# Kernel optimization log

Hardware: AMD Instinct MI355X
Metric: run time of the kernel (lower is better)

The kernel has to match this reference:

```python
import jax, jax.numpy as jnp
import numpy as np

D_MODEL = 768
D_FF = 3072
N_HEADS = 12
HEAD_DIM = D_MODEL // N_HEADS
SUB_SCALE = 0.5
LN_EPS = 1e-5


def _layer_norm(x, g, b):
    mu = jnp.mean(x, axis=-1, keepdims=True)
    var = jnp.var(x, axis=-1, keepdims=True)
    return (x - mu) * jax.lax.rsqrt(var + LN_EPS) * g + b


def setup_inputs() -> dict:
    key = jax.random.key(0)
    ks = jax.random.split(key, 12)
    B, T = 1, 4096
    s = lambda fan_in: 1.0 / np.sqrt(fan_in)
    return {
        "x": jax.random.normal(ks[0], (B, T, D_MODEL), dtype=jnp.float32),
        "ln1_g": jnp.ones((D_MODEL,), jnp.float32),
        "ln1_b": jnp.zeros((D_MODEL,), jnp.float32),
        "ln2_g": jnp.ones((D_MODEL,), jnp.float32),
        "ln2_b": jnp.zeros((D_MODEL,), jnp.float32),
        "qkv_w": jax.random.normal(ks[1], (D_MODEL, 3 * D_MODEL), jnp.float32) * s(D_MODEL),
        "qkv_b": jnp.zeros((3 * D_MODEL,), jnp.float32),
        "out_w": jax.random.normal(ks[2], (D_MODEL, D_MODEL), jnp.float32) * s(D_MODEL),
        "out_b": jnp.zeros((D_MODEL,), jnp.float32),
        "fc1_w": jax.random.normal(ks[3], (D_MODEL, D_FF), jnp.float32) * s(D_MODEL),
        "fc1_b": jnp.zeros((D_FF,), jnp.float32),
        "fc2_w": jax.random.normal(ks[4], (D_FF, D_MODEL), jnp.float32) * s(D_FF),
        "fc2_b": jnp.zeros((D_MODEL,), jnp.float32),
    }


def reference(x, ln1_g, ln1_b, ln2_g, ln2_b, qkv_w, qkv_b, out_w, out_b,
              fc1_w, fc1_b, fc2_w, fc2_b):
    B, T, C = x.shape
    # --- attention sub-block ---
    h = _layer_norm(x, ln1_g, ln1_b) * SUB_SCALE
    qkv = h @ qkv_w + qkv_b                      # [B,T,3C]
    q, k, v = jnp.split(qkv, 3, axis=-1)
    split = lambda t: t.reshape(B, T, N_HEADS, HEAD_DIM).transpose(0, 2, 1, 3)
    q, k, v = split(q), split(k), split(v)       # [B,H,T,Hd]
    scores = jnp.einsum('bhqd,bhkd->bhqk', q, k) / jnp.sqrt(jnp.float32(HEAD_DIM))
    weights = jax.nn.softmax(scores, axis=-1)    # [B,H,T,T] (no mask, as in source)
    attn = jnp.einsum('bhqk,bhkd->bhqd', weights, v)
    attn = attn.transpose(0, 2, 1, 3).reshape(B, T, C)
    x = x + attn @ out_w + out_b
    # --- MLP sub-block ---
    h2 = _layer_norm(x, ln2_g, ln2_b) * SUB_SCALE
    h2 = jax.nn.gelu(h2 @ fc1_w + fc1_b, approximate=False)  # nn.GELU() = exact erf
    h2 = h2 @ fc2_w + fc2_b
    return x + h2
```

## Files before the change

kernel.cpp:

```cpp
#include <hip/hip_runtime.h>
#include <hip/hip_bf16.h>
#include <math.h>

#define TSEQ 4096
#define DMODEL 768
#define DFF 3072
#define NHEADS 12
#define HDIM 64

typedef __attribute__((ext_vector_type(8))) short short8;
typedef __attribute__((ext_vector_type(4))) short bf16x4;
typedef __attribute__((ext_vector_type(4))) float f32x4;
typedef unsigned short ushort;
typedef unsigned int uint;

typedef __attribute__((address_space(1))) ushort as1_ushort;
typedef __attribute__((address_space(3))) ushort as3_ushort;

__device__ __forceinline__ void gl_lds16(const ushort* g, const ushort* l) {
    __builtin_amdgcn_global_load_lds((as1_ushort*)(uintptr_t)g,
                                     (as3_ushort*)(uint)(uintptr_t)l, 16, 0, 0);
}

__device__ __forceinline__ ushort f2bf(float f) {
    union { float f; unsigned i; } c; c.f = f;
    unsigned x = c.i;
    unsigned r = x + 0x7FFFu + ((x >> 16) & 1u);
    return (ushort)(r >> 16);
}
__device__ __forceinline__ float asf(uint u) {
    union { unsigned i; float f; } c; c.i = u; return c.f;
}

__global__ __launch_bounds__(256) void ln_half_kernel(
    const float* __restrict__ x, const float* __restrict__ g,
    const float* __restrict__ b, ushort* __restrict__ out)
{
    int row = blockIdx.x;
    const float* xr = x + (size_t)row * DMODEL;
    float v[3];
    float s = 0.f, s2 = 0.f;
    #pragma unroll
    for (int i = 0; i < 3; i++) {
        v[i] = xr[threadIdx.x + 256 * i];
        s += v[i]; s2 += v[i] * v[i];
    }
    #pragma unroll
    for (int m = 1; m < 64; m <<= 1) { s += __shfl_xor(s, m, 64); s2 += __shfl_xor(s2, m, 64); }
    __shared__ float ss[4], ss2[4];
    int wid = threadIdx.x >> 6;
    if ((threadIdx.x & 63) == 0) { ss[wid] = s; ss2[wid] = s2; }
    __syncthreads();
    s = ss[0] + ss[1] + ss[2] + ss[3];
    s2 = ss2[0] + ss2[1] + ss2[2] + ss2[3];
    float mu = s * (1.f / DMODEL);
    float var = s2 * (1.f / DMODEL) - mu * mu;
    float rs = rsqrtf(var + 1e-5f);
    #pragma unroll
    for (int i = 0; i < 3; i++) {
        int c = threadIdx.x + 256 * i;
        float h = (v[i] - mu) * rs * g[c] + b[c];
        out[(size_t)row * DMODEL + c] = f2bf(h * 0.5f);
    }
}

__global__ __launch_bounds__(256) void transpose_cast_kernel(
    const float* __restrict__ in, ushort* __restrict__ out, int K, int N)
{
    __shared__ float tile[32][33];
    int k0 = blockIdx.x * 32, n0 = blockIdx.y * 32;
    int c = threadIdx.x & 31, r0 = threadIdx.x >> 5;
    #pragma unroll
    for (int i = 0; i < 4; i++) {
        int r = r0 + i * 8;
        tile[r][c] = in[(size_t)(k0 + r) * N + n0 + c];
    }
    __syncthreads();
    #pragma unroll
    for (int i = 0; i < 4; i++) {
        int r = r0 + i * 8;
        out[(size_t)(n0 + r) * K + k0 + c] = f2bf(tile[c][r]);
    }
}

template<int EPI>
__global__ __launch_bounds__(256) void gemm_kernel(
    const ushort* __restrict__ A, const ushort* __restrict__ Bt,
    const float* __restrict__ bias, const float* __restrict__ res,
    void* __restrict__ out, int M, int N, int K)
{
    __shared__ ushort As[3][128 * 32];
    __shared__ ushort Bs[3][128 * 32];
    int bm = blockIdx.x * 128, bn = blockIdx.y * 128;
    int tid = threadIdx.x;
    int wid = tid >> 6, lane = tid & 63;
    int wm = (wid >> 1) * 64, wn = (wid & 1) * 64;
    int lg = lane >> 4, lr = lane & 15;
    int srow = lane >> 2, scol = (lane & 3) * 8;
    f32x4 acc[4][4] = {};

    const ushort* ga0 = A  + (size_t)(bm + wid * 16 + srow) * K + scol;
    const ushort* ga1 = A  + (size_t)(bm + 64 + wid * 16 + srow) * K + scol;
    const ushort* gb0 = Bt + (size_t)(bn + wid * 16 + srow) * K + scol;
    const ushort* gb1 = Bt + (size_t)(bn + 64 + wid * 16 + srow) * K + scol;

    auto STAGE = [&](int t, int b) {
        int k0 = t << 5;
        gl_lds16(ga0 + k0, &As[b][wid * 512]);
        gl_lds16(ga1 + k0, &As[b][2048 + wid * 512]);
        gl_lds16(gb0 + k0, &Bs[b][wid * 512]);
        gl_lds16(gb1 + k0, &Bs[b][2048 + wid * 512]);
    };

    int nt = K >> 5;
    STAGE(0, 0);
    STAGE(1, 1);

    int cur = 0;
    for (int t = 0; t < nt; t++) {
        if (t + 1 < nt) { asm volatile("s_waitcnt vmcnt(4)" ::: "memory"); }
        else            { asm volatile("s_waitcnt vmcnt(0)" ::: "memory"); }
        __builtin_amdgcn_s_barrier();
        if (t + 2 < nt) STAGE(t + 2, cur == 0 ? 2 : cur - 1);
        short8 a[4], b[4];
        #pragma unroll
        for (int mi = 0; mi < 4; mi++) a[mi] = *(const short8*)&As[cur][(wm + mi * 16 + lr) * 32 + lg * 8];
        #pragma unroll
        for (int ni = 0; ni < 4; ni++) b[ni] = *(const short8*)&Bs[cur][(wn + ni * 16 + lr) * 32 + lg * 8];
        #pragma unroll
        for (int mi = 0; mi < 4; mi++)
            #pragma unroll
            for (int ni = 0; ni < 4; ni++)
                acc[mi][ni] = __builtin_amdgcn_mfma_f32_16x16x32_bf16(a[mi], b[ni], acc[mi][ni], 0, 0, 0);
        cur = (cur == 2) ? 0 : cur + 1;
    }

    #pragma unroll
    for (int mi = 0; mi < 4; mi++) {
        #pragma unroll
        for (int ni = 0; ni < 4; ni++) {
            int col = bn + wn + ni * 16 + lr;
            float bv = bias[col];
            #pragma unroll
            for (int r = 0; r < 4; r++) {
                int row = bm + wm + mi * 16 + lg * 4 + r;
                float v = acc[mi][ni][r] + bv;
                size_t idx = (size_t)row * N + col;
                if (EPI == 0) {
                    ((ushort*)out)[idx] = f2bf(v);
                } else if (EPI == 1) {
                    float gv = 0.5f * v * (1.f + erff(v * 0.70710678118f));
                    ((ushort*)out)[idx] = f2bf(gv);
                } else {
                    ((float*)out)[idx] = v + res[idx];
                }
            }
        }
    }
}

__global__ __launch_bounds__(512) void attn_kernel(
    const ushort* __restrict__ qkv, ushort* __restrict__ Opart, float* __restrict__ ml)
{
    int h = blockIdx.y;
    int qb = blockIdx.x;
    int split = blockIdx.z;
    __shared__ ushort Ks[2][64 * 64];
    __shared__ ushort Vt[2][64 * 72];
    __shared__ ushort Ps[128 * 72];
    int tid = threadIdx.x, wid = tid >> 6, lane = tid & 63;
    int lg = lane >> 4, lr = lane & 15;
    const float C1 = 0.18033688011112042f;
    const float KC = 12.0f * C1;
    const size_t sbase = (size_t)split * 1024 * 2304;

    {
        int row = tid >> 2, cc = (tid & 3) * 16;
        const ushort* src = qkv + (size_t)(qb * 128 + row) * 2304 + h * HDIM + cc;
        *(short8*)&Ps[row * 72 + cc]     = *(const short8*)src;
        *(short8*)&Ps[row * 72 + cc + 8] = *(const short8*)(src + 8);
    }
    int prow = (wid * 16 + lr) * 72;
    short8 qf0 = *(const short8*)&Ps[prow + lg * 8];
    short8 qf1 = *(const short8*)&Ps[prow + 32 + lg * 8];

    short8 vone;
    #pragma unroll
    for (int i = 0; i < 8; i++) vone[i] = (short)0x3F80;

    int krow = tid >> 3;
    int kunit = (tid & 7) ^ (krow & 7);
    const ushort* kg = qkv + sbase + (size_t)krow * 2304 + DMODEL + h * HDIM + kunit * 8;
    int va_ = tid & 31, dg = tid >> 5;
    const ushort* vg = qkv + sbase + (size_t)(2 * va_) * 2304 + 2 * DMODEL + h * HDIM + dg * 4;

    bf16x4 nva = *(const bf16x4*)vg;
    bf16x4 nvb = *(const bf16x4*)(vg + 2304);
    gl_lds16(kg, &Ks[0][tid * 8]);
    #pragma unroll
    for (int i = 0; i < 4; i++) {
        uint pk = ((uint)(ushort)nva[i]) | (((uint)(ushort)nvb[i]) << 16);
        *(uint*)&Vt[0][(dg * 4 + i) * 72 + va_ * 2] = pk;
    }

    f32x4 o[4] = {};
    f32x4 o5 = {};
    const int NT = 16;
    int x7 = lr & 7;

    for (int kt = 0; kt < NT; kt++) {
        int cur = kt & 1, nb = cur ^ 1;
        bool pf = (kt + 1 < NT);
        __syncthreads();
        if (pf) {
            size_t off = (size_t)(kt + 1) * 64 * 2304;
            nva = *(const bf16x4*)(vg + off);
            nvb = *(const bf16x4*)(vg + off + 2304);
            gl_lds16(kg + off, &Ks[nb][tid * 8]);
        }

        f32x4 st[4] = {};
        #pragma unroll
        for (int ki = 0; ki < 4; ki++) {
            const ushort* kr = &Ks[cur][(ki * 16 + lr) * 64];
            short8 k0 = *(const short8*)&kr[(lg ^ x7) * 8];
            short8 k1 = *(const short8*)&kr[((4 + lg) ^ x7) * 8];
            st[ki] = __builtin_amdgcn_mfma_f32_16x16x32_bf16(k0, qf0, st[ki], 0, 0, 0);
            st[ki] = __builtin_amdgcn_mfma_f32_16x16x32_bf16(k1, qf1, st[ki], 0, 0, 0);
        }

        #pragma unroll
        for (int ki = 0; ki < 4; ki++)
            #pragma unroll
            for (int r = 0; r < 4; r++)
                st[ki][r] = exp2f(st[ki][r] * C1 - KC);

        #pragma unroll
        for (int ki = 0; ki < 4; ki++) {
            uint d0, d1;
            asm("v_cvt_pk_bf16_f32 %0, %1, %2" : "=v"(d0) : "v"(st[ki][0]), "v"(st[ki][1]));
            asm("v_cvt_pk_bf16_f32 %0, %1, %2" : "=v"(d1) : "v"(st[ki][2]), "v"(st[ki][3]));
            *(uint*)&Ps[prow + ki * 16 + lg * 4]     = d0;
            *(uint*)&Ps[prow + ki * 16 + lg * 4 + 2] = d1;
        }

        short8 pa0 = *(const short8*)&Ps[prow + lg * 8];
        short8 pa1 = *(const short8*)&Ps[prow + 32 + lg * 8];
        o5 = __builtin_amdgcn_mfma_f32_16x16x32_bf16(pa0, vone, o5, 0, 0, 0);
        o5 = __builtin_amdgcn_mfma_f32_16x16x32_bf16(pa1, vone, o5, 0, 0, 0);
        #pragma unroll
        for (int ni = 0; ni < 4; ni++) {
            const ushort* vr = &Vt[cur][(ni * 16 + lr) * 72];
            short8 b0 = *(const short8*)&vr[lg * 8];
            short8 b1 = *(const short8*)&vr[32 + lg * 8];
            o[ni] = __builtin_amdgcn_mfma_f32_16x16x32_bf16(pa0, b0, o[ni], 0, 0, 0);
            o[ni] = __builtin_amdgcn_mfma_f32_16x16x32_bf16(pa1, b1, o[ni], 0, 0, 0);
        }

        if (pf) {
            #pragma unroll
            for (int i = 0; i < 4; i++) {
                uint pk = ((uint)(ushort)nva[i]) | (((uint)(ushort)nvb[i]) << 16);
                *(uint*)&Vt[nb][(dg * 4 + i) * 72 + va_ * 2] = pk;
            }
        }
    }

    if (lr == 0) {
        #pragma unroll
        for (int r = 0; r < 4; r++) {
            int q = qb * 128 + wid * 16 + lg * 4 + r;
            ml[((size_t)split * NHEADS + h) * TSEQ + q] = o5[r];
        }
    }
    #pragma unroll
    for (int ni = 0; ni < 4; ni++)
        #pragma unroll
        for (int r = 0; r < 4; r++) {
            int qrow = qb * 128 + wid * 16 + lg * 4 + r;
            int dcol = ni * 16 + lr;
            Opart[((size_t)split * TSEQ + qrow) * DMODEL + h * HDIM + dcol] = f2bf(o[ni][r]);
        }
}

__global__ __launch_bounds__(256) void attn_combine_kernel(
    const ushort* __restrict__ Opart, const float* __restrict__ ml,
    ushort* __restrict__ attnb)
{
    int gid = blockIdx.x * 256 + threadIdx.x;
    int q = gid / 192;
    int c = (gid - q * 192) * 4;
    int hh = c >> 6;
    float denom = 0.f;
    float a0 = 0.f, a1 = 0.f, a2 = 0.f, a3 = 0.f;
    #pragma unroll
    for (int s = 0; s < 4; s++) {
        denom += ml[((size_t)s * NHEADS + hh) * TSEQ + q];
        uint2 ov = *(const uint2*)&Opart[((size_t)s * TSEQ + q) * DMODEL + c];
        a0 += asf(ov.x << 16);
        a1 += asf(ov.x & 0xFFFF0000u);
        a2 += asf(ov.y << 16);
        a3 += asf(ov.y & 0xFFFF0000u);
    }
    float rd = 1.f / denom;
    uint2 stv;
    stv.x = (uint)f2bf(a0 * rd) | ((uint)f2bf(a1 * rd) << 16);
    stv.y = (uint)f2bf(a2 * rd) | ((uint)f2bf(a3 * rd) << 16);
    *(uint2*)&attnb[(size_t)q * DMODEL + c] = stv;
}

extern "C" void kernel_launch(void* const* d_in, const int* in_sizes, int n_in,
                              void* d_out, int out_size, void* d_ws, size_t ws_size,
                              hipStream_t stream)
{
    const float* x      = (const float*)d_in[0];
    const float* ln1_g  = (const float*)d_in[1];
    const float* ln1_b  = (const float*)d_in[2];
    const float* ln2_g  = (const float*)d_in[3];
    const float* ln2_b  = (const float*)d_in[4];
    const float* qkv_w  = (const float*)d_in[5];
    const float* qkv_b  = (const float*)d_in[6];
    const float* out_w  = (const float*)d_in[7];
    const float* out_b  = (const float*)d_in[8];
    const float* fc1_w  = (const float*)d_in[9];
    const float* fc1_b  = (const float*)d_in[10];
    const float* fc2_w  = (const float*)d_in[11];
    const float* fc2_b  = (const float*)d_in[12];
    (void)in_sizes; (void)n_in; (void)out_size; (void)ws_size;

    char* p = (char*)d_ws;
    ushort* qkvb  = (ushort*)p;                 p += (size_t)TSEQ * DFF * 2;
    ushort* hb    = (ushort*)p;                 p += (size_t)TSEQ * DMODEL * 2;
    ushort* attnb = (ushort*)p;                 p += (size_t)TSEQ * DMODEL * 2;
    float*  x2    = (float*)p;                  p += (size_t)TSEQ * DMODEL * 4;
    ushort* qkv_wT = (ushort*)p;                p += (size_t)(3 * DMODEL) * DMODEL * 2;
    ushort* out_wT = (ushort*)p;                p += (size_t)DMODEL * DMODEL * 2;
    ushort* fc1_wT = (ushort*)p;                p += (size_t)DFF * DMODEL * 2;
    ushort* fc2_wT = (ushort*)p;                p += (size_t)DMODEL * DFF * 2;
    ushort* Opart  = (ushort*)p;                p += (size_t)4 * TSEQ * DMODEL * 2;
    float*  mlbuf  = (float*)p;                 p += (size_t)4 * NHEADS * TSEQ * 4;
    ushort* gb = qkvb;

    transpose_cast_kernel<<<dim3(DMODEL / 32, 3 * DMODEL / 32), 256, 0, stream>>>(qkv_w, qkv_wT, DMODEL, 3 * DMODEL);
    transpose_cast_kernel<<<dim3(DMODEL / 32, DMODEL / 32), 256, 0, stream>>>(out_w, out_wT, DMODEL, DMODEL);
    transpose_cast_kernel<<<dim3(DMODEL / 32, DFF / 32), 256, 0, stream>>>(fc1_w, fc1_wT, DMODEL, DFF);
    transpose_cast_kernel<<<dim3(DFF / 32, DMODEL / 32), 256, 0, stream>>>(fc2_w, fc2_wT, DFF, DMODEL);

    ln_half_kernel<<<TSEQ, 256, 0, stream>>>(x, ln1_g, ln1_b, hb);
    gemm_kernel<0><<<dim3(TSEQ / 128, 3 * DMODEL / 128), 256, 0, stream>>>(
        hb, qkv_wT, qkv_b, nullptr, qkvb, TSEQ, 3 * DMODEL, DMODEL);
    attn_kernel<<<dim3(TSEQ / 128, NHEADS, 4), 512, 0, stream>>>(qkvb, Opart, mlbuf);
    attn_combine_kernel<<<(TSEQ * DMODEL / 4) / 256, 256, 0, stream>>>(Opart, mlbuf, attnb);
    gemm_kernel<2><<<dim3(TSEQ / 128, DMODEL / 128), 256, 0, stream>>>(
        attnb, out_wT, out_b, x, x2, TSEQ, DMODEL, DMODEL);
    ln_half_kernel<<<TSEQ, 256, 0, stream>>>(x2, ln2_g, ln2_b, hb);
    gemm_kernel<1><<<dim3(TSEQ / 128, DFF / 128), 256, 0, stream>>>(
        hb, fc1_wT, fc1_b, nullptr, gb, TSEQ, DFF, DMODEL);
    gemm_kernel<2><<<dim3(TSEQ / 128, DMODEL / 128), 256, 0, stream>>>(
        gb, fc2_wT, fc2_b, x2, (float*)d_out, TSEQ, DMODEL, DFF);
}
```

Baseline: 238.4 us.

## Pre-transpose V for attention, add N64 GEMMs, tanh GELU, double-buffer GEMM

A separate kernel now writes V transposed into a workspace buffer, so attention can load V tiles straight into LDS (with an XOR swizzle) instead of repacking registers every iteration. The two GEMMs with N=768 switch to a 128x64 tile variant, which launches more blocks to fill the GPU better. The GEMM pipeline drops from three LDS buffers to two, with a plain __syncthreads per step. The exact erf GELU is replaced by a tanh-style approximation computed with exp2 and a hardware reciprocal. The tanh form changes numerics slightly, the extra transpose adds a launch and memory traffic, and the shallower pipeline may expose more load latency.

```diff
diff --git a/kernel.cpp b/kernel.cpp
--- a/kernel.cpp
+++ b/kernel.cpp
@@ -9,7 +9,6 @@
 #define HDIM 64
 
 typedef __attribute__((ext_vector_type(8))) short short8;
-typedef __attribute__((ext_vector_type(4))) short bf16x4;
 typedef __attribute__((ext_vector_type(4))) float f32x4;
 typedef unsigned short ushort;
 typedef unsigned int uint;
@@ -30,6 +29,13 @@
 }
 __device__ __forceinline__ float asf(uint u) {
     union { unsigned i; float f; } c; c.i = u; return c.f;
+}
+__device__ __forceinline__ float gelu_fast(float v) {
+    float y = v * (0.7978845608f + 0.03567740814f * v * v);
+    float u = exp2f(y * -2.8853900817779268f);
+    float r;
+    asm("v_rcp_f32 %0, %1" : "=v"(r) : "v"(1.f + u));
+    return v * r;
 }
 
 __global__ __launch_bounds__(256) void ln_half_kernel(
@@ -83,14 +89,36 @@
     }
 }
 
+__global__ __launch_bounds__(256) void vtrans_kernel(
+    const ushort* __restrict__ qkvb, ushort* __restrict__ vT)
+{
+    __shared__ ushort tile[64][72];
+    int t0 = blockIdx.x * 64, d0 = blockIdx.y * 64;
+    int tid = threadIdx.x;
+    int r = tid >> 2, c = (tid & 3) * 16;
+    const ushort* src = qkvb + (size_t)(t0 + r) * 2304 + 1536 + d0 + c;
+    *(short8*)&tile[r][c]     = *(const short8*)src;
+    *(short8*)&tile[r][c + 8] = *(const short8*)(src + 8);
+    __syncthreads();
+    int d = tid & 63, gq = tid >> 6;
+    short8 w0, w1;
+    #pragma unroll
+    for (int i = 0; i < 8; i++) w0[i] = (short)tile[gq * 16 + i][d];
+    #pragma unroll
+    for (int i = 0; i < 8; i++) w1[i] = (short)tile[gq * 16 + 8 + i][d];
+    ushort* dst = vT + (size_t)(d0 + d) * TSEQ + t0 + gq * 16;
+    *(short8*)dst       = w0;
+    *(short8*)(dst + 8) = w1;
+}
+
 template<int EPI>
 __global__ __launch_bounds__(256) void gemm_kernel(
     const ushort* __restrict__ A, const ushort* __restrict__ Bt,
     const float* __restrict__ bias, const float* __restrict__ res,
     void* __restrict__ out, int M, int N, int K)
 {
-    __shared__ ushort As[3][128 * 32];
-    __shared__ ushort Bs[3][128 * 32];
+    __shared__ ushort As[2][128 * 32];
+    __shared__ ushort Bs[2][128 * 32];
     int bm = blockIdx.x * 128, bn = blockIdx.y * 128;
     int tid = threadIdx.x;
     int wid = tid >> 6, lane = tid & 63;
@@ -104,24 +132,23 @@
     const ushort* gb0 = Bt + (size_t)(bn + wid * 16 + srow) * K + scol;
     const ushort* gb1 = Bt + (size_t)(bn + 64 + wid * 16 + srow) * K + scol;
 
-    auto STAGE = [&](int t, int b) {
-        int k0 = t << 5;
-        gl_lds16(ga0 + k0, &As[b][wid * 512]);
-        gl_lds16(ga1 + k0, &As[b][2048 + wid * 512]);
-        gl_lds16(gb0 + k0, &Bs[b][wid * 512]);
-        gl_lds16(gb1 + k0, &Bs[b][2048 + wid * 512]);
-    };
+    gl_lds16(ga0, &As[0][wid * 512]);
+    gl_lds16(ga1, &As[0][2048 + wid * 512]);
+    gl_lds16(gb0, &Bs[0][wid * 512]);
+    gl_lds16(gb1, &Bs[0][2048 + wid * 512]);
 
     int nt = K >> 5;
-    STAGE(0, 0);
-    STAGE(1, 1);
-
-    int cur = 0;
     for (int t = 0; t < nt; t++) {
-        if (t + 1 < nt) { asm volatile("s_waitcnt vmcnt(4)" ::: "memory"); }
-        else            { asm volatile("s_waitcnt vmcnt(0)" ::: "memory"); }
-        __builtin_amdgcn_s_barrier();
-        if (t + 2 < nt) STAGE(t + 2, cur == 0 ? 2 : cur - 1);
+        int cur = t & 1;
+        __syncthreads();
+        if (t + 1 < nt) {
+            int k0 = (t + 1) << 5;
+            int nb = cur ^ 1;
+            gl_lds16(ga0 + k0, &As[nb][wid * 512]);
+            gl_lds16(ga1 + k0, &As[nb][2048 + wid * 512]);
+            gl_lds16(gb0 + k0, &Bs[nb][wid * 512]);
+            gl_lds16(gb1 + k0, &Bs[nb][2048 + wid * 512]);
+        }
         short8 a[4], b[4];
         #pragma unroll
         for (int mi = 0; mi < 4; mi++) a[mi] = *(const short8*)&As[cur][(wm + mi * 16 + lr) * 32 + lg * 8];
@@ -132,7 +159,6 @@
             #pragma unroll
             for (int ni = 0; ni < 4; ni++)
                 acc[mi][ni] = __builtin_amdgcn_mfma_f32_16x16x32_bf16(a[mi], b[ni], acc[mi][ni], 0, 0, 0);
-        cur = (cur == 2) ? 0 : cur + 1;
     }
 
     #pragma unroll
@@ -149,8 +175,7 @@
                 if (EPI == 0) {
                     ((ushort*)out)[idx] = f2bf(v);
                 } else if (EPI == 1) {
-                    float gv = 0.5f * v * (1.f + erff(v * 0.70710678118f));
-                    ((ushort*)out)[idx] = f2bf(gv);
+                    ((ushort*)out)[idx] = f2bf(gelu_fast(v));
                 } else {
                     ((float*)out)[idx] = v + res[idx];
                 }
@@ -159,20 +184,90 @@
     }
 }
 
+template<int EPI>
+__global__ __launch_bounds__(256) void gemm_n64_kernel(
+    const ushort* __restrict__ A, const ushort* __restrict__ Bt,
+    const float* __restrict__ bias, const float* __restrict__ res,
+    void* __restrict__ out, int M, int N, int K)
+{
+    __shared__ ushort As[2][128 * 32];
+    __shared__ ushort Bs[2][64 * 32];
+    int bm = blockIdx.x * 128, bn = blockIdx.y * 64;
+    int tid = threadIdx.x;
+    int wid = tid >> 6, lane = tid & 63;
+    int wm = (wid >> 1) * 64, wn = (wid & 1) * 32;
+    int lg = lane >> 4, lr = lane & 15;
+    int srow = lane >> 2, scol = (lane & 3) * 8;
+    f32x4 acc[4][2] = {};
+
+    const ushort* ga0 = A  + (size_t)(bm + wid * 16 + srow) * K + scol;
+    const ushort* ga1 = A  + (size_t)(bm + 64 + wid * 16 + srow) * K + scol;
+    const ushort* gb0 = Bt + (size_t)(bn + wid * 16 + srow) * K + scol;
+
+    gl_lds16(ga0, &As[0][wid * 512]);
+    gl_lds16(ga1, &As[0][2048 + wid * 512]);
+    gl_lds16(gb0, &Bs[0][wid * 512]);
+
+    int nt = K >> 5;
+    for (int t = 0; t < nt; t++) {
+        int cur = t & 1;
+        __syncthreads();
+        if (t + 1 < nt) {
+            int k0 = (t + 1) << 5;
+            int nb = cur ^ 1;
+            gl_lds16(ga0 + k0, &As[nb][wid * 512]);
+            gl_lds16(ga1 + k0, &As[nb][2048 + wid * 512]);
+            gl_lds16(gb0 + k0, &Bs[nb][wid * 512]);
+        }
+        short8 a[4], b[2];
+        #pragma unroll
+        for (int mi = 0; mi < 4; mi++) a[mi] = *(const short8*)&As[cur][(wm + mi * 16 + lr) * 32 + lg * 8];
+        #pragma unroll
+        for (int ni = 0; ni < 2; ni++) b[ni] = *(const short8*)&Bs[cur][(wn + ni * 16 + lr) * 32 + lg * 8];
+        #pragma unroll
+        for (int mi = 0; mi < 4; mi++)
+            #pragma unroll
+            for (int ni = 0; ni < 2; ni++)
+                acc[mi][ni] = __builtin_amdgcn_mfma_f32_16x16x32_bf16(a[mi], b[ni], acc[mi][ni], 0, 0, 0);
+    }
+
+    #pragma unroll
+    for (int mi = 0; mi < 4; mi++) {
+        #pragma unroll
+        for (int ni = 0; ni < 2; ni++) {
+            int col = bn + wn + ni * 16 + lr;
+            float bv = bias[col];
+            #pragma unroll
+            for (int r = 0; r < 4; r++) {
+                int row = bm + wm + mi * 16 + lg * 4 + r;
+                float v = acc[mi][ni][r] + bv;
+                size_t idx = (size_t)row * N + col;
+                if (EPI == 0) {
+                    ((ushort*)out)[idx] = f2bf(v);
+                } else if (EPI == 1) {
+                    ((ushort*)out)[idx] = f2bf(gelu_fast(v));
+                } else {
+                    ((float*)out)[idx] = v + res[idx];
+                }
+            }
+        }
+    }
+}
+
 __global__ __launch_bounds__(512) void attn_kernel(
-    const ushort* __restrict__ qkv, ushort* __restrict__ Opart, float* __restrict__ ml)
+    const ushort* __restrict__ qkv, const ushort* __restrict__ vT,
+    ushort* __restrict__ Opart, float* __restrict__ ml)
 {
     int h = blockIdx.y;
     int qb = blockIdx.x;
     int split = blockIdx.z;
     __shared__ ushort Ks[2][64 * 64];
-    __shared__ ushort Vt[2][64 * 72];
+    __shared__ ushort Vt[2][64 * 64];
     __shared__ ushort Ps[128 * 72];
     int tid = threadIdx.x, wid = tid >> 6, lane = tid & 63;
     int lg = lane >> 4, lr = lane & 15;
     const float C1 = 0.18033688011112042f;
     const float KC = 12.0f * C1;
-    const size_t sbase = (size_t)split * 1024 * 2304;
 
     {
         int row = tid >> 2, cc = (tid & 3) * 16;
@@ -190,18 +285,11 @@
 
     int krow = tid >> 3;
     int kunit = (tid & 7) ^ (krow & 7);
-    const ushort* kg = qkv + sbase + (size_t)krow * 2304 + DMODEL + h * HDIM + kunit * 8;
-    int va_ = tid & 31, dg = tid >> 5;
-    const ushort* vg = qkv + sbase + (size_t)(2 * va_) * 2304 + 2 * DMODEL + h * HDIM + dg * 4;
-
-    bf16x4 nva = *(const bf16x4*)vg;
-    bf16x4 nvb = *(const bf16x4*)(vg + 2304);
+    const ushort* kg = qkv + (size_t)(split * 1024 + krow) * 2304 + DMODEL + h * HDIM + kunit * 8;
+    const ushort* vgp = vT + (size_t)(h * HDIM + krow) * TSEQ + split * 1024 + kunit * 8;
+
     gl_lds16(kg, &Ks[0][tid * 8]);
-    #pragma unroll
-    for (int i = 0; i < 4; i++) {
-        uint pk = ((uint)(ushort)nva[i]) | (((uint)(ushort)nvb[i]) << 16);
-        *(uint*)&Vt[0][(dg * 4 + i) * 72 + va_ * 2] = pk;
-    }
+    gl_lds16(vgp, &Vt[0][tid * 8]);
 
     f32x4 o[4] = {};
     f32x4 o5 = {};
@@ -210,13 +298,10 @@
 
     for (int kt = 0; kt < NT; kt++) {
         int cur = kt & 1, nb = cur ^ 1;
-        bool pf = (kt + 1 < NT);
         __syncthreads();
-        if (pf) {
-            size_t off = (size_t)(kt + 1) * 64 * 2304;
-            nva = *(const bf16x4*)(vg + off);
-            nvb = *(const bf16x4*)(vg + off + 2304);
-            gl_lds16(kg + off, &Ks[nb][tid * 8]);
+        if (kt + 1 < NT) {
+            gl_lds16(kg + (size_t)(kt + 1) * 64 * 2304, &Ks[nb][tid * 8]);
+            gl_lds16(vgp + (size_t)(kt + 1) * 64, &Vt[nb][tid * 8]);
         }
 
         f32x4 st[4] = {};
@@ -250,19 +335,11 @@
         o5 = __builtin_amdgcn_mfma_f32_16x16x32_bf16(pa1, vone, o5, 0, 0, 0);
         #pragma unroll
         for (int ni = 0; ni < 4; ni++) {
-            const ushort* vr = &Vt[cur][(ni * 16 + lr) * 72];
-            short8 b0 = *(const short8*)&vr[lg * 8];
-            short8 b1 = *(const short8*)&vr[32 + lg * 8];
+            const ushort* vr = &Vt[cur][(ni * 16 + lr) * 64];
+            short8 b0 = *(const short8*)&vr[(lg ^ x7) * 8];
+            short8 b1 = *(const short8*)&vr[((4 + lg) ^ x7) * 8];
             o[ni] = __builtin_amdgcn_mfma_f32_16x16x32_bf16(pa0, b0, o[ni], 0, 0, 0);
             o[ni] = __builtin_amdgcn_mfma_f32_16x16x32_bf16(pa1, b1, o[ni], 0, 0, 0);
-        }
-
-        if (pf) {
-            #pragma unroll
-            for (int i = 0; i < 4; i++) {
-                uint pk = ((uint)(ushort)nva[i]) | (((uint)(ushort)nvb[i]) << 16);
-                *(uint*)&Vt[nb][(dg * 4 + i) * 72 + va_ * 2] = pk;
-            }
         }
     }
 
@@ -339,6 +416,7 @@
     ushort* fc2_wT = (ushort*)p;                p += (size_t)DMODEL * DFF * 2;
     ushort* Opart  = (ushort*)p;                p += (size_t)4 * TSEQ * DMODEL * 2;
     float*  mlbuf  = (float*)p;                 p += (size_t)4 * NHEADS * TSEQ * 4;
+    ushort* vTb    = (ushort*)p;                p += (size_t)DMODEL * TSEQ * 2;
     ushort* gb = qkvb;
 
     transpose_cast_kernel<<<dim3(DMODEL / 32, 3 * DMODEL / 32), 256, 0, stream>>>(qkv_w, qkv_wT, DMODEL, 3 * DMODEL);
@@ -349,13 +427,14 @@
     ln_half_kernel<<<TSEQ, 256, 0, stream>>>(x, ln1_g, ln1_b, hb);
     gemm_kernel<0><<<dim3(TSEQ / 128, 3 * DMODEL / 128), 256, 0, stream>>>(
         hb, qkv_wT, qkv_b, nullptr, qkvb, TSEQ, 3 * DMODEL, DMODEL);
-    attn_kernel<<<dim3(TSEQ / 128, NHEADS, 4), 512, 0, stream>>>(qkvb, Opart, mlbuf);
+    vtrans_kernel<<<dim3(TSEQ / 64, DMODEL / 64), 256, 0, stream>>>(qkvb, vTb);
+    attn_kernel<<<dim3(TSEQ / 128, NHEADS, 4), 512, 0, stream>>>(qkvb, vTb, Opart, mlbuf);
     attn_combine_kernel<<<(TSEQ * DMODEL / 4) / 256, 256, 0, stream>>>(Opart, mlbuf, attnb);
-    gemm_kernel<2><<<dim3(TSEQ / 128, DMODEL / 128), 256, 0, stream>>>(
+    gemm_n64_kernel<2><<<dim3(TSEQ / 128, DMODEL / 64), 256, 0, stream>>>(
         attnb, out_wT, out_b, x, x2, TSEQ, DMODEL, DMODEL);
     ln_half_kernel<<<TSEQ, 256, 0, stream>>>(x2, ln2_g, ln2_b, hb);
     gemm_kernel<1><<<dim3(TSEQ / 128, DFF / 128), 256, 0, stream>>>(
         hb, fc1_wT, fc1_b, nullptr, gb, TSEQ, DFF, DMODEL);
-    gemm_kernel<2><<<dim3(TSEQ / 128, DMODEL / 128), 256, 0, stream>>>(
+    gemm_n64_kernel<2><<<dim3(TSEQ / 128, DMODEL / 64), 256, 0, stream>>>(
         gb, fc2_wT, fc2_b, x2, (float*)d_out, TSEQ, DMODEL, DFF);
 }
```

Result: faster. 225.8 us (-5.3%).
